# Kernel tuning notes

Measured on AMD Instinct MI355X. Metric: run time of the kernel, lower is better.

Reference implementation:

```python
import jax, jax.numpy as jnp
import numpy as np
from jax import lax

B, DIM, H, W = 4, 128, 56, 56
NH, NG = 4, 2
CG = DIM // NG   # group channels (64)
HC = DIM // NH   # head channels (32)
KS = 7
ORF = 2.0        # offset_range_factor
EPS = 1e-5

def setup_inputs() -> dict:
    key = jax.random.key(0)
    ks = jax.random.split(key, 8)
    s = 0.05
    def rn(k, shp):
        return jax.random.normal(k, shp, jnp.float32) * s
    return {
        "x":    jax.random.normal(ks[0], (B, DIM, H, W), jnp.float32),
        "dw_w": rn(ks[1], (CG, 1, KS, KS)),   # depthwise conv weight
        "dw_b": jnp.zeros((CG,), jnp.float32),
        "ln_g": jnp.ones((CG,), jnp.float32),
        "ln_b": jnp.zeros((CG,), jnp.float32),
        "off_w": rn(ks[2], (2, CG)),          # 1x1 conv to 2 offset channels, no bias
        "q_w": rn(ks[3], (DIM, DIM)), "q_b": jnp.zeros((DIM,), jnp.float32),
        "k_w": rn(ks[4], (DIM, DIM)), "k_b": jnp.zeros((DIM,), jnp.float32),
        "v_w": rn(ks[5], (DIM, DIM)), "v_b": jnp.zeros((DIM,), jnp.float32),
        "o_w": rn(ks[6], (DIM, DIM)), "o_b": jnp.zeros((DIM,), jnp.float32),
    }

def _grid_sample_bilinear(img, grid):
    # img [N,C,Hi,Wi]; grid [N,Ho,Wo,2] with (x,y) in [-1,1]; align_corners=True, zero padding
    N, C, Hi, Wi = img.shape
    Ho, Wo = grid.shape[1], grid.shape[2]
    gx = (grid[..., 0] + 1.0) * 0.5 * (Wi - 1)
    gy = (grid[..., 1] + 1.0) * 0.5 * (Hi - 1)
    x0 = jnp.floor(gx); y0 = jnp.floor(gy)
    wx1 = gx - x0; wx0 = 1.0 - wx1
    wy1 = gy - y0; wy0 = 1.0 - wy1
    flat = img.reshape(N, C, Hi * Wi)
    def corner(xi, yi, w):
        valid = (xi >= 0) & (xi <= Wi - 1) & (yi >= 0) & (yi <= Hi - 1)
        xc = jnp.clip(xi, 0, Wi - 1).astype(jnp.int32)
        yc = jnp.clip(yi, 0, Hi - 1).astype(jnp.int32)
        idx = (yc * Wi + xc).reshape(N, 1, Ho * Wo)
        vals = jnp.take_along_axis(flat, idx, axis=2)
        return vals * (w * valid).reshape(N, 1, Ho * Wo)
    out = (corner(x0, y0, wx0 * wy0) + corner(x0 + 1.0, y0, wx1 * wy0)
           + corner(x0, y0 + 1.0, wx0 * wy1) + corner(x0 + 1.0, y0 + 1.0, wx1 * wy1))
    return out.reshape(N, C, Ho, Wo)

def reference(x, dw_w, dw_b, ln_g, ln_b, off_w, q_w, q_b, k_w, k_b, v_w, v_b, o_w, o_b):
    Bx = x.shape[0]
    # q projection (1x1 conv)
    q = jnp.einsum('oc,bchw->bohw', q_w, x) + q_b[None, :, None, None]
    # offset branch: depthwise conv -> LayerNorm(channels) -> GELU -> 1x1 conv (2 ch)
    q_off = q.reshape(Bx * NG, CG, H, W)
    h = lax.conv_general_dilated(q_off, dw_w, (1, 1), [(KS // 2, KS // 2)] * 2,
                                 feature_group_count=CG,
                                 dimension_numbers=('NCHW', 'OIHW', 'NCHW'))
    h = h + dw_b[None, :, None, None]
    hn = jnp.moveaxis(h, 1, -1)                       # [BG,H,W,CG]
    mu = hn.mean(-1, keepdims=True)
    var = ((hn - mu) ** 2).mean(-1, keepdims=True)
    hn = (hn - mu) * lax.rsqrt(var + EPS) * ln_g + ln_b
    hn = jax.nn.gelu(hn, approximate=False)
    off = jnp.einsum('pc,bhwc->bphw', off_w, hn)      # [BG,2,Hk,Wk], p=(y,x)
    Hk, Wk = off.shape[2], off.shape[3]
    n = Hk * Wk
    rng = jnp.array([1.0 / Hk, 1.0 / Wk], jnp.float32).reshape(1, 2, 1, 1)
    off = jnp.tanh(off) * rng * ORF
    off = jnp.moveaxis(off, 1, -1)                    # [BG,Hk,Wk,2]
    # normalized reference points (y,x)
    ry = (jnp.arange(Hk, dtype=jnp.float32) + 0.5) / Hk * 2.0 - 1.0
    rx = (jnp.arange(Wk, dtype=jnp.float32) + 0.5) / Wk * 2.0 - 1.0
    ref = jnp.stack(jnp.meshgrid(ry, rx, indexing='ij'), -1)  # [Hk,Wk,2]
    pos = off + ref[None]
    # deformable gather: grid_sample expects (x,y)
    xs = _grid_sample_bilinear(x.reshape(Bx * NG, CG, H, W), pos[..., ::-1])
    xs = xs.reshape(Bx, DIM, n)                       # group-major == channel layout
    k = jnp.einsum('oc,bcn->bon', k_w, xs) + k_b[None, :, None]
    v = jnp.einsum('oc,bcn->bon', v_w, xs) + v_b[None, :, None]
    qh = q.reshape(Bx * NH, HC, H * W)
    kh = k.reshape(Bx * NH, HC, n)
    vh = v.reshape(Bx * NH, HC, n)
    attn = jnp.einsum('bcm,bcn->bmn', qh, kh) * (HC ** -0.5)
    attn = jax.nn.softmax(attn, axis=2)
    out = jnp.einsum('bmn,bcn->bcm', attn, vh).reshape(Bx, DIM, H, W)
    return jnp.einsum('oc,bchw->bohw', o_w, out) + o_b[None, :, None, None]
```

## Files before the change

### kernel.cpp

```cpp
#include <hip/hip_runtime.h>
#include <hip/hip_bf16.h>

#define HW 3136

typedef short s16x8 __attribute__((ext_vector_type(8)));
typedef float f32x4 __attribute__((ext_vector_type(4)));
typedef unsigned short us4 __attribute__((ext_vector_type(4)));
typedef unsigned short us8 __attribute__((ext_vector_type(8)));

__device__ inline unsigned short f2bf(float f) {
  union { float f; unsigned int u; } v; v.f = f;
  unsigned int r = v.u + 0x7fff + ((v.u >> 16) & 1);
  return (unsigned short)(r >> 16);
}
__device__ inline float bf2f(unsigned short b) {
  union { unsigned int u; float f; } v; v.u = (unsigned int)b << 16;
  return v.f;
}

__global__ __launch_bounds__(256) void wconv_kernel(
    const float* __restrict__ w0, const float* __restrict__ w1,
    const float* __restrict__ w2, const float* __restrict__ w3,
    unsigned short* __restrict__ o0, unsigned short* __restrict__ o1,
    unsigned short* __restrict__ o2, unsigned short* __restrict__ o3h,
    unsigned short* __restrict__ o3l) {
  int i = blockIdx.x * 256 + threadIdx.x;
  int y = blockIdx.y;
  if (y < 3) {
    const float* s = (y == 0) ? w0 : (y == 1) ? w1 : w2;
    unsigned short* d = (y == 0) ? o0 : (y == 1) ? o1 : o2;
    d[i] = f2bf(s[i]);
  } else {
    float x = w3[i];
    unsigned short hi = f2bf(x);
    o3h[i] = hi;
    o3l[i] = f2bf(x - bf2f(hi));
  }
}

__global__ __launch_bounds__(128) void gemm_q_kernel(
    const float* __restrict__ x, const unsigned short* __restrict__ Wq,
    const float* __restrict__ bias, float* __restrict__ Outf,
    unsigned short* __restrict__ Outb) {
  int by = blockIdx.y;
  int b = by >> 1, oh = by & 1;
  int t = threadIdx.x;
  int w = t >> 6, l = t & 63;
  int lq = l & 15, h = l >> 4;
  int p = blockIdx.x * 32 + w * 16 + lq;

  union S8 { s16x8 v; unsigned short u[8]; };
  S8 bfr[4];
  const float* xs = x + (size_t)b * 128 * HW + p;
  #pragma unroll
  for (int k = 0; k < 4; ++k)
    #pragma unroll
    for (int j = 0; j < 8; ++j)
      bfr[k].u[j] = f2bf(xs[(size_t)(k * 32 + h * 8 + j) * HW]);

  f32x4 acc[4] = {};
  #pragma unroll
  for (int k = 0; k < 4; ++k) {
    #pragma unroll
    for (int ot = 0; ot < 4; ++ot) {
      int og = oh * 4 + ot;
      s16x8 af = *(const s16x8*)&Wq[(size_t)(og * 16 + lq) * 128 + k * 32 + h * 8];
      acc[ot] = __builtin_amdgcn_mfma_f32_16x16x32_bf16(af, bfr[k].v, acc[ot], 0, 0, 0);
    }
  }

  size_t cb = (size_t)b * 128 * HW;
  #pragma unroll
  for (int ot = 0; ot < 4; ++ot) {
    int og = oh * 4 + ot;
    float4 bv = *(const float4*)&bias[og * 16 + h * 4];
    float r[4] = {acc[ot][0] + bv.x, acc[ot][1] + bv.y,
                  acc[ot][2] + bv.z, acc[ot][3] + bv.w};
    #pragma unroll
    for (int i = 0; i < 4; ++i)
      Outf[cb + (size_t)(og * 16 + h * 4 + i) * HW + p] = r[i];
    const float S = 0.25503968151135f;
    us4 rb;
    #pragma unroll
    for (int i = 0; i < 4; ++i) rb[i] = f2bf(r[i] * S);
    *(us4*)&Outb[((size_t)b * HW + p) * 128 + og * 16 + h * 4] = rb;
  }
}

__global__ __launch_bounds__(128) void gemm_kv_kernel(
    const unsigned short* __restrict__ InT, const unsigned short* __restrict__ Wk,
    const unsigned short* __restrict__ Wv, const float* __restrict__ k_b,
    const float* __restrict__ v_b, unsigned short* __restrict__ kbT,
    unsigned short* __restrict__ vb) {
  int by = blockIdx.y;
  int b = by >> 1, oh = by & 1;
  int t = threadIdx.x;
  int w = t >> 6, l = t & 63;
  int lq = l & 15, h = l >> 4;
  int p = blockIdx.x * 32 + w * 16 + lq;

  s16x8 bfr[4];
  const unsigned short* bsrc = InT + ((size_t)b * HW + p) * 128 + h * 8;
  #pragma unroll
  for (int k = 0; k < 4; ++k) bfr[k] = *(const s16x8*)&bsrc[k * 32];

  {
    f32x4 acc[4] = {};
    #pragma unroll
    for (int k = 0; k < 4; ++k) {
      #pragma unroll
      for (int ot = 0; ot < 4; ++ot) {
        int og = oh * 4 + ot;
        s16x8 af = *(const s16x8*)&Wk[(size_t)(og * 16 + lq) * 128 + k * 32 + h * 8];
        acc[ot] = __builtin_amdgcn_mfma_f32_16x16x32_bf16(af, bfr[k], acc[ot], 0, 0, 0);
      }
    }
    #pragma unroll
    for (int ot = 0; ot < 4; ++ot) {
      int og = oh * 4 + ot;
      float4 bv = *(const float4*)&k_b[og * 16 + h * 4];
      us4 rb;
      #pragma unroll
      for (int i = 0; i < 4; ++i) rb[i] = f2bf(acc[ot][i] + bv[i]);
      *(us4*)&kbT[((size_t)b * HW + p) * 128 + og * 16 + h * 4] = rb;
    }
  }
  {
    f32x4 acc[4] = {};
    #pragma unroll
    for (int k = 0; k < 4; ++k) {
      #pragma unroll
      for (int ot = 0; ot < 4; ++ot) {
        int og = oh * 4 + ot;
        s16x8 af = *(const s16x8*)&Wv[(size_t)(og * 16 + lq) * 128 + k * 32 + h * 8];
        acc[ot] = __builtin_amdgcn_mfma_f32_16x16x32_bf16(af, bfr[k], acc[ot], 0, 0, 0);
      }
    }
    size_t cb = (size_t)b * 128 * HW;
    #pragma unroll
    for (int ot = 0; ot < 4; ++ot) {
      int og = oh * 4 + ot;
      float4 bv = *(const float4*)&v_b[og * 16 + h * 4];
      #pragma unroll
      for (int i = 0; i < 4; ++i)
        vb[cb + (size_t)(og * 16 + h * 4 + i) * HW + p] = f2bf(acc[ot][i] + bv[i]);
    }
  }
}

__global__ __launch_bounds__(128) void o_gemm_kernel(
    const unsigned short* __restrict__ AHi, const unsigned short* __restrict__ ALo,
    const unsigned short* __restrict__ WHi, const unsigned short* __restrict__ WLo,
    const float* __restrict__ bias, float* __restrict__ Outf) {
  int by = blockIdx.y;
  int b = by >> 1, oh = by & 1;
  int t = threadIdx.x;
  int w = t >> 6, l = t & 63;
  int lq = l & 15, h = l >> 4;
  int p = blockIdx.x * 32 + w * 16 + lq;

  s16x8 bH[4], bL[4];
  const unsigned short* bsH = AHi + ((size_t)b * HW + p) * 128 + h * 8;
  const unsigned short* bsL = ALo + ((size_t)b * HW + p) * 128 + h * 8;
  #pragma unroll
  for (int k = 0; k < 4; ++k) {
    bH[k] = *(const s16x8*)&bsH[k * 32];
    bL[k] = *(const s16x8*)&bsL[k * 32];
  }

  f32x4 acc[4] = {};
  #pragma unroll
  for (int k = 0; k < 4; ++k) {
    #pragma unroll
    for (int ot = 0; ot < 4; ++ot) {
      int og = oh * 4 + ot;
      size_t wi = (size_t)(og * 16 + lq) * 128 + k * 32 + h * 8;
      s16x8 aH = *(const s16x8*)&WHi[wi];
      s16x8 aL = *(const s16x8*)&WLo[wi];
      acc[ot] = __builtin_amdgcn_mfma_f32_16x16x32_bf16(aH, bH[k], acc[ot], 0, 0, 0);
      acc[ot] = __builtin_amdgcn_mfma_f32_16x16x32_bf16(aH, bL[k], acc[ot], 0, 0, 0);
      acc[ot] = __builtin_amdgcn_mfma_f32_16x16x32_bf16(aL, bH[k], acc[ot], 0, 0, 0);
    }
  }

  size_t cb = (size_t)b * 128 * HW;
  #pragma unroll
  for (int ot = 0; ot < 4; ++ot) {
    int og = oh * 4 + ot;
    float4 bv = *(const float4*)&bias[og * 16 + h * 4];
    #pragma unroll
    for (int i = 0; i < 4; ++i)
      Outf[cb + (size_t)(og * 16 + h * 4 + i) * HW + p] = acc[ot][i] + bv[i];
  }
}

__global__ __launch_bounds__(1024) void offset_kernel(
    const float* __restrict__ q, const float* __restrict__ dw_w,
    const float* __restrict__ dw_b, const float* __restrict__ ln_g,
    const float* __restrict__ ln_b, const float* __restrict__ off_w,
    float* __restrict__ pos) {
  __shared__ float vs[64][65];
  __shared__ float mu_s[64], rs_s[64];
  __shared__ float part[16][64][2];
  int bg = blockIdx.x, h = blockIdx.y;
  int t = threadIdx.x;
  int w = t & 63;
  int cq = t >> 6;
  int b = bg >> 1, g = bg & 1;
  const float* qb = q + ((size_t)b * 128 + (size_t)g * 64) * HW;

  #pragma unroll
  for (int i = 0; i < 4; ++i) {
    int c = cq * 4 + i;
    float acc = dw_b[c];
    const float* qc = qb + (size_t)c * HW;
    const float* wc = dw_w + c * 49;
    #pragma unroll
    for (int ky = 0; ky < 7; ++ky) {
      int y = h + ky - 3;
      if (y >= 0 && y < 56) {
        #pragma unroll
        for (int kx = 0; kx < 7; ++kx) {
          int xx = w + kx - 3;
          if (xx >= 0 && xx < 56)
            acc += qc[y * 56 + xx] * wc[ky * 7 + kx];
        }
      }
    }
    vs[c][w] = acc;
  }
  __syncthreads();

  if (cq == 0) {
    float sum = 0.f;
    #pragma unroll 8
    for (int c = 0; c < 64; ++c) sum += vs[c][w];
    float mu = sum * 0.015625f;
    float var = 0.f;
    #pragma unroll 8
    for (int c = 0; c < 64; ++c) { float d = vs[c][w] - mu; var += d * d; }
    mu_s[w] = mu;
    rs_s[w] = rsqrtf(var * 0.015625f + 1e-5f);
  }
  __syncthreads();

  {
    float mu = mu_s[w], rstd = rs_s[w];
    float oy = 0.f, ox = 0.f;
    #pragma unroll
    for (int i = 0; i < 4; ++i) {
      int c = cq * 4 + i;
      float hn = (vs[c][w] - mu) * rstd * ln_g[c] + ln_b[c];
      hn = 0.5f * hn * (1.f + erff(hn * 0.70710678118654752f));
      oy += off_w[c] * hn;
      ox += off_w[64 + c] * hn;
    }
    part[cq][w][0] = oy;
    part[cq][w][1] = ox;
  }
  __syncthreads();

  if (cq == 0 && w < 56) {
    float oy = 0.f, ox = 0.f;
    #pragma unroll
    for (int pw = 0; pw < 16; ++pw) {
      oy += part[pw][w][0];
      ox += part[pw][w][1];
    }
    float py = tanhf(oy) * (2.0f / 56.f) + ((h + 0.5f) * (2.f / 56.f) - 1.f);
    float px = tanhf(ox) * (2.0f / 56.f) + ((w + 0.5f) * (2.f / 56.f) - 1.f);
    int idx = bg * HW + h * 56 + w;
    pos[idx * 2 + 0] = (px + 1.f) * 0.5f * 55.f;
    pos[idx * 2 + 1] = (py + 1.f) * 0.5f * 55.f;
  }
}

__global__ __launch_bounds__(256) void sample_kernel(
    const float* __restrict__ x, const float* __restrict__ pos,
    unsigned short* __restrict__ xsT) {
  int t = threadIdx.x;
  int p = blockIdx.x * 64 + (t & 63);
  int cg = t >> 6;
  int bg = p / HW, pp = p % HW;
  int b = bg >> 1, g = bg & 1;
  float gx = pos[2 * p], gy = pos[2 * p + 1];
  float x0f = floorf(gx), y0f = floorf(gy);
  float wx1 = gx - x0f, wx0 = 1.f - wx1;
  float wy1 = gy - y0f, wy0 = 1.f - wy1;
  int x0 = (int)x0f, y0 = (int)y0f;
  int x1 = x0 + 1, y1 = y0 + 1;
  float vx0 = (x0 >= 0 && x0 < 56) ? 1.f : 0.f;
  float vx1 = (x1 >= 0 && x1 < 56) ? 1.f : 0.f;
  float vy0 = (y0 >= 0 && y0 < 56) ? 1.f : 0.f;
  float vy1 = (y1 >= 0 && y1 < 56) ? 1.f : 0.f;
  int xc0 = min(max(x0, 0), 55), xc1 = min(max(x1, 0), 55);
  int yc0 = min(max(y0, 0), 55), yc1 = min(max(y1, 0), 55);
  float w00 = wx0 * wy0 * vx0 * vy0, w10 = wx1 * wy0 * vx1 * vy0;
  float w01 = wx0 * wy1 * vx0 * vy1, w11 = wx1 * wy1 * vx1 * vy1;
  int i00 = yc0 * 56 + xc0, i10 = yc0 * 56 + xc1;
  int i01 = yc1 * 56 + xc0, i11 = yc1 * 56 + xc1;
  const float* xb = x + ((size_t)b * 128 + (size_t)g * 64 + cg * 16) * HW;
  unsigned short tmp[16];
  #pragma unroll 4
  for (int i = 0; i < 16; ++i) {
    const float* xc = xb + (size_t)i * HW;
    tmp[i] = f2bf(w00 * xc[i00] + w10 * xc[i10] + w01 * xc[i01] + w11 * xc[i11]);
  }
  unsigned short* dst = xsT + ((size_t)b * HW + pp) * 128 + g * 64 + cg * 16;
  *(us8*)&dst[0] = *(us8*)&tmp[0];
  *(us8*)&dst[8] = *(us8*)&tmp[8];
}

__global__ __launch_bounds__(128) void attn_mfma_kernel(
    const unsigned short* __restrict__ qT, const unsigned short* __restrict__ kT,
    const unsigned short* __restrict__ vbf, unsigned short* __restrict__ aoHi,
    unsigned short* __restrict__ aoLo) {
  __shared__ __align__(16) unsigned short Klds[2][64][40];
  __shared__ __align__(16) unsigned short Plds[2][2][16][68];
  const int KSTEP = 64 * 40;
  int bh = blockIdx.y;
  int b = bh >> 2, hd = bh & 3;
  int t = threadIdx.x;
  int w = t >> 6, l = t & 63;
  int lq = l & 15, h = l >> 4;
  int q0 = blockIdx.x * 64 + w * 32;
  size_t vbase = (size_t)bh * 32 * HW;

  union S8 { s16x8 v; long long q[2]; unsigned short u[8]; };

  S8 qf0, qf1;
  qf0.v = *(const s16x8*)&qT[((size_t)b * HW + q0 + lq) * 128 + hd * 32 + h * 8];
  qf1.v = *(const s16x8*)&qT[((size_t)b * HW + q0 + 16 + lq) * 128 + hd * 32 + h * 8];

  int srow = t >> 1, sseg = (t & 1) * 16;
  const unsigned short* ksrc =
      kT + ((size_t)b * HW + srow) * 128 + hd * 32 + sseg;
  unsigned short* kdst = &Klds[0][srow][sseg];

  const unsigned short* vl = vbf + vbase + (size_t)lq * HW + h * 8;

  f32x4 oacc0[2] = {{0.f, 0.f, 0.f, 0.f}, {0.f, 0.f, 0.f, 0.f}};
  f32x4 oacc1[2] = {{0.f, 0.f, 0.f, 0.f}, {0.f, 0.f, 0.f, 0.f}};
  float lsum0 = 0.f, lsum1 = 0.f;

  S8 kr0, kr1, vreg[4];
  kr0.v = *(const s16x8*)&ksrc[0];
  kr1.v = *(const s16x8*)&ksrc[8];
  *(s16x8*)&kdst[0] = kr0.v;
  *(s16x8*)&kdst[8] = kr1.v;
  kr0.v = *(const s16x8*)&ksrc[(size_t)64 * 128];
  kr1.v = *(const s16x8*)&ksrc[(size_t)64 * 128 + 8];
  #pragma unroll
  for (int c = 0; c < 2; ++c)
    #pragma unroll
    for (int n = 0; n < 2; ++n)
      vreg[c * 2 + n].v = *(const s16x8*)&vl[(size_t)(n * 16) * HW + c * 32];
  asm volatile("s_waitcnt lgkmcnt(0)" ::: "memory");
  __builtin_amdgcn_s_barrier();

  for (int tix = 0; tix < 49; ++tix) {
    int cur = tix & 1;
    int kbV = (tix + 1 < 49) ? (tix + 1) * 64 : 0;
    int kbK = (tix + 2 < 49) ? (tix + 2) * 64 : 3072;

    f32x4 st0[4], st1[4];
    #pragma unroll
    for (int tt = 0; tt < 4; ++tt) {
      S8 af;
      af.v = *(const s16x8*)&Klds[cur][tt * 16 + lq][h * 8];
      st0[tt] = __builtin_amdgcn_mfma_f32_16x16x32_bf16(
          af.v, qf0.v, (f32x4){0.f, 0.f, 0.f, 0.f}, 0, 0, 0);
      st1[tt] = __builtin_amdgcn_mfma_f32_16x16x32_bf16(
          af.v, qf1.v, (f32x4){0.f, 0.f, 0.f, 0.f}, 0, 0, 0);
    }

    #pragma unroll
    for (int tt = 0; tt < 4; ++tt) {
      float a0, a1, a2, a3, b0, b1, b2, b3;
      asm("v_exp_f32 %0, %1" : "=v"(a0) : "v"(st0[tt][0]));
      asm("v_exp_f32 %0, %1" : "=v"(a1) : "v"(st0[tt][1]));
      asm("v_exp_f32 %0, %1" : "=v"(a2) : "v"(st0[tt][2]));
      asm("v_exp_f32 %0, %1" : "=v"(a3) : "v"(st0[tt][3]));
      asm("v_exp_f32 %0, %1" : "=v"(b0) : "v"(st1[tt][0]));
      asm("v_exp_f32 %0, %1" : "=v"(b1) : "v"(st1[tt][1]));
      asm("v_exp_f32 %0, %1" : "=v"(b2) : "v"(st1[tt][2]));
      asm("v_exp_f32 %0, %1" : "=v"(b3) : "v"(st1[tt][3]));
      lsum0 += (a0 + a1) + (a2 + a3);
      lsum1 += (b0 + b1) + (b2 + b3);
      unsigned int lo0, hi0, lo1, hi1;
      asm("v_cvt_pk_bf16_f32 %0, %1, %2" : "=v"(lo0) : "v"(a0), "v"(a1));
      asm("v_cvt_pk_bf16_f32 %0, %1, %2" : "=v"(hi0) : "v"(a2), "v"(a3));
      asm("v_cvt_pk_bf16_f32 %0, %1, %2" : "=v"(lo1) : "v"(b0), "v"(b1));
      asm("v_cvt_pk_bf16_f32 %0, %1, %2" : "=v"(hi1) : "v"(b2), "v"(b3));
      unsigned long long pk0 = (unsigned long long)lo0 | ((unsigned long long)hi0 << 32);
      unsigned long long pk1 = (unsigned long long)lo1 | ((unsigned long long)hi1 << 32);
      *(unsigned long long*)&Plds[w][0][lq][tt * 16 + h * 4] = pk0;
      *(unsigned long long*)&Plds[w][1][lq][tt * 16 + h * 4] = pk1;
    }

    #pragma unroll
    for (int c = 0; c < 2; ++c) {
      S8 pf0, pf1;
      pf0.q[0] = *(const long long*)&Plds[w][0][lq][c * 32 + h * 8];
      pf0.q[1] = *(const long long*)&Plds[w][0][lq][c * 32 + h * 8 + 4];
      pf1.q[0] = *(const long long*)&Plds[w][1][lq][c * 32 + h * 8];
      pf1.q[1] = *(const long long*)&Plds[w][1][lq][c * 32 + h * 8 + 4];
      #pragma unroll
      for (int n = 0; n < 2; ++n) {
        oacc0[n] = __builtin_amdgcn_mfma_f32_16x16x32_bf16(
            vreg[c * 2 + n].v, pf0.v, oacc0[n], 0, 0, 0);
        oacc1[n] = __builtin_amdgcn_mfma_f32_16x16x32_bf16(
            vreg[c * 2 + n].v, pf1.v, oacc1[n], 0, 0, 0);
      }
    }

    #pragma unroll
    for (int c = 0; c < 2; ++c)
      #pragma unroll
      for (int n = 0; n < 2; ++n)
        vreg[c * 2 + n].v =
            *(const s16x8*)&vl[(size_t)(n * 16) * HW + kbV + c * 32];

    *(s16x8*)(kdst + (cur ^ 1) * KSTEP) = kr0.v;
    *(s16x8*)(kdst + (cur ^ 1) * KSTEP + 8) = kr1.v;
    kr0.v = *(const s16x8*)&ksrc[(size_t)kbK * 128];
    kr1.v = *(const s16x8*)&ksrc[(size_t)kbK * 128 + 8];

    asm volatile("s_waitcnt lgkmcnt(0)" ::: "memory");
    __builtin_amdgcn_s_barrier();
  }

  lsum0 += __shfl_xor(lsum0, 16);
  lsum0 += __shfl_xor(lsum0, 32);
  lsum1 += __shfl_xor(lsum1, 16);
  lsum1 += __shfl_xor(lsum1, 32);
  float inv0 = 1.f / lsum0;
  float inv1 = 1.f / lsum1;
  #pragma unroll
  for (int f = 0; f < 2; ++f) {
    float inv = f ? inv1 : inv0;
    f32x4* oacc = f ? oacc1 : oacc0;
    size_t obase = ((size_t)b * HW + q0 + f * 16 + lq) * 128 + hd * 32;
    #pragma unroll
    for (int n = 0; n < 2; ++n) {
      us4 rh, rl;
      #pragma unroll
      for (int r = 0; r < 4; ++r) {
        float v = oacc[n][r] * inv;
        unsigned short hi = f2bf(v);
        rh[r] = hi;
        rl[r] = f2bf(v - bf2f(hi));
      }
      *(us4*)&aoHi[obase + n * 16 + h * 4] = rh;
      *(us4*)&aoLo[obase + n * 16 + h * 4] = rl;
    }
  }
}

extern "C" void kernel_launch(void* const* d_in, const int* in_sizes, int n_in,
                              void* d_out, int out_size, void* d_ws, size_t ws_size,
                              hipStream_t stream) {
  const float* x    = (const float*)d_in[0];
  const float* dw_w = (const float*)d_in[1];
  const float* dw_b = (const float*)d_in[2];
  const float* ln_g = (const float*)d_in[3];
  const float* ln_b = (const float*)d_in[4];
  const float* offw = (const float*)d_in[5];
  const float* q_w  = (const float*)d_in[6];
  const float* q_b  = (const float*)d_in[7];
  const float* k_w  = (const float*)d_in[8];
  const float* k_b  = (const float*)d_in[9];
  const float* v_w  = (const float*)d_in[10];
  const float* v_b  = (const float*)d_in[11];
  const float* o_w  = (const float*)d_in[12];
  const float* o_b  = (const float*)d_in[13];

  const size_t NE = 1605632;
  float* ws  = (float*)d_ws;
  float* q   = ws;
  float* pos = q + NE;
  unsigned short* xsT  = (unsigned short*)(pos + 50176);
  unsigned short* qbT  = xsT + NE;
  unsigned short* kbT  = qbT + NE;
  unsigned short* vb   = kbT + NE;
  unsigned short* aoHi = vb + NE;
  unsigned short* aoLo = aoHi + NE;
  unsigned short* Wq   = aoLo + NE;
  unsigned short* Wk   = Wq + 16384;
  unsigned short* Wv   = Wk + 16384;
  unsigned short* WoH  = Wv + 16384;
  unsigned short* WoL  = WoH + 16384;
  float* out = (float*)d_out;

  wconv_kernel<<<dim3(64, 4), 256, 0, stream>>>(q_w, k_w, v_w, o_w,
                                                Wq, Wk, Wv, WoH, WoL);
  gemm_q_kernel<<<dim3(98, 8), 128, 0, stream>>>(x, Wq, q_b, q, qbT);
  offset_kernel<<<dim3(8, 56), 1024, 0, stream>>>(q, dw_w, dw_b, ln_g, ln_b, offw, pos);
  sample_kernel<<<dim3(392), 256, 0, stream>>>(x, pos, xsT);
  gemm_kv_kernel<<<dim3(98, 8), 128, 0, stream>>>(xsT, Wk, Wv, k_b, v_b, kbT, vb);
  attn_mfma_kernel<<<dim3(49, 16), 128, 0, stream>>>(qbT, kbT, vb, aoHi, aoLo);
  o_gemm_kernel<<<dim3(98, 8), 128, 0, stream>>>(aoHi, aoLo, WoH, WoL, o_b, out);
}
```

Baseline: 145.4 us.

## Split attention key range across two wave pairs and merge partial sums in LDS

The attention kernel now launches 256 threads per block. Two pairs of waves each process about half of the 49 key tiles for the same 64 queries, each pair with its own double-buffered K tile in LDS. At the end, one half writes its unnormalized output accumulators and row sums to shared memory, and the other half adds them, normalizes and stores the result. The aim is more waves in flight and a shorter serial loop per wave, which matters because the grid has only 784 blocks. The cost is more LDS, a merge step, and one wasted padded iteration where the second half has no valid tile.

```diff
diff --git a/kernel.cpp b/kernel.cpp
--- a/kernel.cpp
+++ b/kernel.cpp
@@ -311,19 +311,20 @@
   *(us8*)&dst[8] = *(us8*)&tmp[8];
 }
 
-__global__ __launch_bounds__(128) void attn_mfma_kernel(
+__global__ __launch_bounds__(256) void attn_mfma_kernel(
     const unsigned short* __restrict__ qT, const unsigned short* __restrict__ kT,
     const unsigned short* __restrict__ vbf, unsigned short* __restrict__ aoHi,
     unsigned short* __restrict__ aoLo) {
-  __shared__ __align__(16) unsigned short Klds[2][64][40];
-  __shared__ __align__(16) unsigned short Plds[2][2][16][68];
+  __shared__ __align__(16) unsigned short Klds[2][2][64][40];
+  __shared__ __align__(16) unsigned short Plds[4][2][16][68];
   const int KSTEP = 64 * 40;
   int bh = blockIdx.y;
   int b = bh >> 2, hd = bh & 3;
   int t = threadIdx.x;
   int w = t >> 6, l = t & 63;
+  int qg = w >> 1, kh = w & 1;
   int lq = l & 15, h = l >> 4;
-  int q0 = blockIdx.x * 64 + w * 32;
+  int q0 = blockIdx.x * 64 + qg * 32;
   size_t vbase = (size_t)bh * 32 * HW;
 
   union S8 { s16x8 v; long long q[2]; unsigned short u[8]; };
@@ -332,10 +333,11 @@
   qf0.v = *(const s16x8*)&qT[((size_t)b * HW + q0 + lq) * 128 + hd * 32 + h * 8];
   qf1.v = *(const s16x8*)&qT[((size_t)b * HW + q0 + 16 + lq) * 128 + hd * 32 + h * 8];
 
-  int srow = t >> 1, sseg = (t & 1) * 16;
+  int pid = qg * 64 + l;
+  int srow = pid >> 1, sseg = (pid & 1) * 16;
   const unsigned short* ksrc =
       kT + ((size_t)b * HW + srow) * 128 + hd * 32 + sseg;
-  unsigned short* kdst = &Klds[0][srow][sseg];
+  unsigned short* kdst = &Klds[kh][0][srow][sseg];
 
   const unsigned short* vl = vbf + vbase + (size_t)lq * HW + h * 8;
 
@@ -343,74 +345,84 @@
   f32x4 oacc1[2] = {{0.f, 0.f, 0.f, 0.f}, {0.f, 0.f, 0.f, 0.f}};
   float lsum0 = 0.f, lsum1 = 0.f;
 
+  int tbase = kh * 25;
+
   S8 kr0, kr1, vreg[4];
-  kr0.v = *(const s16x8*)&ksrc[0];
-  kr1.v = *(const s16x8*)&ksrc[8];
-  *(s16x8*)&kdst[0] = kr0.v;
-  *(s16x8*)&kdst[8] = kr1.v;
-  kr0.v = *(const s16x8*)&ksrc[(size_t)64 * 128];
-  kr1.v = *(const s16x8*)&ksrc[(size_t)64 * 128 + 8];
-  #pragma unroll
-  for (int c = 0; c < 2; ++c)
-    #pragma unroll
-    for (int n = 0; n < 2; ++n)
-      vreg[c * 2 + n].v = *(const s16x8*)&vl[(size_t)(n * 16) * HW + c * 32];
+  {
+    size_t o0 = (size_t)(tbase * 64) * 128;
+    kr0.v = *(const s16x8*)&ksrc[o0];
+    kr1.v = *(const s16x8*)&ksrc[o0 + 8];
+    *(s16x8*)&kdst[0] = kr0.v;
+    *(s16x8*)&kdst[8] = kr1.v;
+    size_t o1 = (size_t)(min(tbase + 1, 48) * 64) * 128;
+    kr0.v = *(const s16x8*)&ksrc[o1];
+    kr1.v = *(const s16x8*)&ksrc[o1 + 8];
+    #pragma unroll
+    for (int c = 0; c < 2; ++c)
+      #pragma unroll
+      for (int n = 0; n < 2; ++n)
+        vreg[c * 2 + n].v =
+            *(const s16x8*)&vl[(size_t)(n * 16) * HW + tbase * 64 + c * 32];
+  }
   asm volatile("s_waitcnt lgkmcnt(0)" ::: "memory");
   __builtin_amdgcn_s_barrier();
 
-  for (int tix = 0; tix < 49; ++tix) {
-    int cur = tix & 1;
-    int kbV = (tix + 1 < 49) ? (tix + 1) * 64 : 0;
-    int kbK = (tix + 2 < 49) ? (tix + 2) * 64 : 3072;
-
-    f32x4 st0[4], st1[4];
-    #pragma unroll
-    for (int tt = 0; tt < 4; ++tt) {
-      S8 af;
-      af.v = *(const s16x8*)&Klds[cur][tt * 16 + lq][h * 8];
-      st0[tt] = __builtin_amdgcn_mfma_f32_16x16x32_bf16(
-          af.v, qf0.v, (f32x4){0.f, 0.f, 0.f, 0.f}, 0, 0, 0);
-      st1[tt] = __builtin_amdgcn_mfma_f32_16x16x32_bf16(
-          af.v, qf1.v, (f32x4){0.f, 0.f, 0.f, 0.f}, 0, 0, 0);
-    }
-
-    #pragma unroll
-    for (int tt = 0; tt < 4; ++tt) {
-      float a0, a1, a2, a3, b0, b1, b2, b3;
-      asm("v_exp_f32 %0, %1" : "=v"(a0) : "v"(st0[tt][0]));
-      asm("v_exp_f32 %0, %1" : "=v"(a1) : "v"(st0[tt][1]));
-      asm("v_exp_f32 %0, %1" : "=v"(a2) : "v"(st0[tt][2]));
-      asm("v_exp_f32 %0, %1" : "=v"(a3) : "v"(st0[tt][3]));
-      asm("v_exp_f32 %0, %1" : "=v"(b0) : "v"(st1[tt][0]));
-      asm("v_exp_f32 %0, %1" : "=v"(b1) : "v"(st1[tt][1]));
-      asm("v_exp_f32 %0, %1" : "=v"(b2) : "v"(st1[tt][2]));
-      asm("v_exp_f32 %0, %1" : "=v"(b3) : "v"(st1[tt][3]));
-      lsum0 += (a0 + a1) + (a2 + a3);
-      lsum1 += (b0 + b1) + (b2 + b3);
-      unsigned int lo0, hi0, lo1, hi1;
-      asm("v_cvt_pk_bf16_f32 %0, %1, %2" : "=v"(lo0) : "v"(a0), "v"(a1));
-      asm("v_cvt_pk_bf16_f32 %0, %1, %2" : "=v"(hi0) : "v"(a2), "v"(a3));
-      asm("v_cvt_pk_bf16_f32 %0, %1, %2" : "=v"(lo1) : "v"(b0), "v"(b1));
-      asm("v_cvt_pk_bf16_f32 %0, %1, %2" : "=v"(hi1) : "v"(b2), "v"(b3));
-      unsigned long long pk0 = (unsigned long long)lo0 | ((unsigned long long)hi0 << 32);
-      unsigned long long pk1 = (unsigned long long)lo1 | ((unsigned long long)hi1 << 32);
-      *(unsigned long long*)&Plds[w][0][lq][tt * 16 + h * 4] = pk0;
-      *(unsigned long long*)&Plds[w][1][lq][tt * 16 + h * 4] = pk1;
-    }
-
-    #pragma unroll
-    for (int c = 0; c < 2; ++c) {
-      S8 pf0, pf1;
-      pf0.q[0] = *(const long long*)&Plds[w][0][lq][c * 32 + h * 8];
-      pf0.q[1] = *(const long long*)&Plds[w][0][lq][c * 32 + h * 8 + 4];
-      pf1.q[0] = *(const long long*)&Plds[w][1][lq][c * 32 + h * 8];
-      pf1.q[1] = *(const long long*)&Plds[w][1][lq][c * 32 + h * 8 + 4];
-      #pragma unroll
-      for (int n = 0; n < 2; ++n) {
-        oacc0[n] = __builtin_amdgcn_mfma_f32_16x16x32_bf16(
-            vreg[c * 2 + n].v, pf0.v, oacc0[n], 0, 0, 0);
-        oacc1[n] = __builtin_amdgcn_mfma_f32_16x16x32_bf16(
-            vreg[c * 2 + n].v, pf1.v, oacc1[n], 0, 0, 0);
+  for (int i = 0; i < 25; ++i) {
+    int cur = i & 1;
+    bool vld = (tbase + i) < 49;
+    int tV = min(tbase + i + 1, 48) * 64;
+    int tK = min(tbase + i + 2, 48) * 64;
+
+    if (vld) {
+      f32x4 st0[4], st1[4];
+      #pragma unroll
+      for (int tt = 0; tt < 4; ++tt) {
+        S8 af;
+        af.v = *(const s16x8*)&Klds[kh][cur][tt * 16 + lq][h * 8];
+        st0[tt] = __builtin_amdgcn_mfma_f32_16x16x32_bf16(
+            af.v, qf0.v, (f32x4){0.f, 0.f, 0.f, 0.f}, 0, 0, 0);
+        st1[tt] = __builtin_amdgcn_mfma_f32_16x16x32_bf16(
+            af.v, qf1.v, (f32x4){0.f, 0.f, 0.f, 0.f}, 0, 0, 0);
+      }
+
+      #pragma unroll
+      for (int tt = 0; tt < 4; ++tt) {
+        float a0, a1, a2, a3, b0, b1, b2, b3;
+        asm("v_exp_f32 %0, %1" : "=v"(a0) : "v"(st0[tt][0]));
+        asm("v_exp_f32 %0, %1" : "=v"(a1) : "v"(st0[tt][1]));
+        asm("v_exp_f32 %0, %1" : "=v"(a2) : "v"(st0[tt][2]));
+        asm("v_exp_f32 %0, %1" : "=v"(a3) : "v"(st0[tt][3]));
+        asm("v_exp_f32 %0, %1" : "=v"(b0) : "v"(st1[tt][0]));
+        asm("v_exp_f32 %0, %1" : "=v"(b1) : "v"(st1[tt][1]));
+        asm("v_exp_f32 %0, %1" : "=v"(b2) : "v"(st1[tt][2]));
+        asm("v_exp_f32 %0, %1" : "=v"(b3) : "v"(st1[tt][3]));
+        lsum0 += (a0 + a1) + (a2 + a3);
+        lsum1 += (b0 + b1) + (b2 + b3);
+        unsigned int lo0, hi0, lo1, hi1;
+        asm("v_cvt_pk_bf16_f32 %0, %1, %2" : "=v"(lo0) : "v"(a0), "v"(a1));
+        asm("v_cvt_pk_bf16_f32 %0, %1, %2" : "=v"(hi0) : "v"(a2), "v"(a3));
+        asm("v_cvt_pk_bf16_f32 %0, %1, %2" : "=v"(lo1) : "v"(b0), "v"(b1));
+        asm("v_cvt_pk_bf16_f32 %0, %1, %2" : "=v"(hi1) : "v"(b2), "v"(b3));
+        unsigned long long pk0 = (unsigned long long)lo0 | ((unsigned long long)hi0 << 32);
+        unsigned long long pk1 = (unsigned long long)lo1 | ((unsigned long long)hi1 << 32);
+        *(unsigned long long*)&Plds[w][0][lq][tt * 16 + h * 4] = pk0;
+        *(unsigned long long*)&Plds[w][1][lq][tt * 16 + h * 4] = pk1;
+      }
+
+      #pragma unroll
+      for (int c = 0; c < 2; ++c) {
+        S8 pf0, pf1;
+        pf0.q[0] = *(const long long*)&Plds[w][0][lq][c * 32 + h * 8];
+        pf0.q[1] = *(const long long*)&Plds[w][0][lq][c * 32 + h * 8 + 4];
+        pf1.q[0] = *(const long long*)&Plds[w][1][lq][c * 32 + h * 8];
+        pf1.q[1] = *(const long long*)&Plds[w][1][lq][c * 32 + h * 8 + 4];
+        #pragma unroll
+        for (int n = 0; n < 2; ++n) {
+          oacc0[n] = __builtin_amdgcn_mfma_f32_16x16x32_bf16(
+              vreg[c * 2 + n].v, pf0.v, oacc0[n], 0, 0, 0);
+          oacc1[n] = __builtin_amdgcn_mfma_f32_16x16x32_bf16(
+              vreg[c * 2 + n].v, pf1.v, oacc1[n], 0, 0, 0);
+        }
       }
     }
 
@@ -419,12 +431,12 @@
       #pragma unroll
       for (int n = 0; n < 2; ++n)
         vreg[c * 2 + n].v =
-            *(const s16x8*)&vl[(size_t)(n * 16) * HW + kbV + c * 32];
-
-    *(s16x8*)(kdst + (cur ^ 1) * KSTEP) = kr0.v;
-    *(s16x8*)(kdst + (cur ^ 1) * KSTEP + 8) = kr1.v;
-    kr0.v = *(const s16x8*)&ksrc[(size_t)kbK * 128];
-    kr1.v = *(const s16x8*)&ksrc[(size_t)kbK * 128 + 8];
+            *(const s16x8*)&vl[(size_t)(n * 16) * HW + tV + c * 32];
+
+    *(s16x8*)(kdst + ((i + 1) & 1) * KSTEP) = kr0.v;
+    *(s16x8*)(kdst + ((i + 1) & 1) * KSTEP + 8) = kr1.v;
+    kr0.v = *(const s16x8*)&ksrc[(size_t)tK * 128];
+    kr1.v = *(const s16x8*)&ksrc[(size_t)tK * 128 + 8];
 
     asm volatile("s_waitcnt lgkmcnt(0)" ::: "memory");
     __builtin_amdgcn_s_barrier();
@@ -434,25 +446,45 @@
   lsum0 += __shfl_xor(lsum0, 32);
   lsum1 += __shfl_xor(lsum1, 16);
   lsum1 += __shfl_xor(lsum1, 32);
-  float inv0 = 1.f / lsum0;
-  float inv1 = 1.f / lsum1;
-  #pragma unroll
-  for (int f = 0; f < 2; ++f) {
-    float inv = f ? inv1 : inv0;
-    f32x4* oacc = f ? oacc1 : oacc0;
-    size_t obase = ((size_t)b * HW + q0 + f * 16 + lq) * 128 + hd * 32;
-    #pragma unroll
-    for (int n = 0; n < 2; ++n) {
-      us4 rh, rl;
-      #pragma unroll
-      for (int r = 0; r < 4; ++r) {
-        float v = oacc[n][r] * inv;
-        unsigned short hi = f2bf(v);
-        rh[r] = hi;
-        rl[r] = f2bf(v - bf2f(hi));
-      }
-      *(us4*)&aoHi[obase + n * 16 + h * 4] = rh;
-      *(us4*)&aoLo[obase + n * 16 + h * 4] = rl;
+
+  float* fb = (float*)&Klds[0][0][0][0];
+  if (kh == 1) {
+    #pragma unroll
+    for (int f = 0; f < 2; ++f) {
+      f32x4* oacc = f ? oacc1 : oacc0;
+      #pragma unroll
+      for (int n = 0; n < 2; ++n)
+        *(f32x4*)&fb[((qg * 2 + f) * 2 + n) * 320 + lq * 20 + h * 4] = oacc[n];
+    }
+    if (h == 0) {
+      fb[2560 + qg * 32 + lq] = lsum0;
+      fb[2560 + qg * 32 + 16 + lq] = lsum1;
+    }
+  }
+  asm volatile("s_waitcnt lgkmcnt(0)" ::: "memory");
+  __builtin_amdgcn_s_barrier();
+
+  if (kh == 0) {
+    #pragma unroll
+    for (int f = 0; f < 2; ++f) {
+      float lsum = (f ? lsum1 : lsum0) + fb[2560 + qg * 32 + f * 16 + lq];
+      float inv = 1.f / lsum;
+      f32x4* oacc = f ? oacc1 : oacc0;
+      size_t obase = ((size_t)b * HW + q0 + f * 16 + lq) * 128 + hd * 32;
+      #pragma unroll
+      for (int n = 0; n < 2; ++n) {
+        f32x4 rem = *(const f32x4*)&fb[((qg * 2 + f) * 2 + n) * 320 + lq * 20 + h * 4];
+        us4 rh, rl;
+        #pragma unroll
+        for (int r = 0; r < 4; ++r) {
+          float v = (oacc[n][r] + rem[r]) * inv;
+          unsigned short hi = f2bf(v);
+          rh[r] = hi;
+          rl[r] = f2bf(v - bf2f(hi));
+        }
+        *(us4*)&aoHi[obase + n * 16 + h * 4] = rh;
+        *(us4*)&aoLo[obase + n * 16 + h * 4] = rl;
+      }
     }
   }
 }
@@ -498,6 +530,6 @@
   offset_kernel<<<dim3(8, 56), 1024, 0, stream>>>(q, dw_w, dw_b, ln_g, ln_b, offw, pos);
   sample_kernel<<<dim3(392), 256, 0, stream>>>(x, pos, xsT);
   gemm_kv_kernel<<<dim3(98, 8), 128, 0, stream>>>(xsT, Wk, Wv, k_b, v_b, kbT, vb);
-  attn_mfma_kernel<<<dim3(49, 16), 128, 0, stream>>>(qbT, kbT, vb, aoHi, aoLo);
+  attn_mfma_kernel<<<dim3(49, 16), 256, 0, stream>>>(qbT, kbT, vb, aoHi, aoLo);
   o_gemm_kernel<<<dim3(98, 8), 128, 0, stream>>>(aoHi, aoLo, WoH, WoL, o_b, out);
 }
```

New measurement: 151.4 us. 1.04x slower.

## Use single-wave attention blocks processing 64 queries without barriers

Applied to the files above, without the earlier changes.

The attention kernel now runs one 64-thread wave per block handling four 16-query fragments instead of two waves of two fragments each. Each wave loads the whole K tile row into LDS itself, so the per-iteration workgroup barrier and LDS wait are removed, and K/V fragments are reused across more queries. The trade-off is half as many waves in flight and higher register use for the larger accumulator set, which may reduce latency hiding.

```diff
diff --git a/kernel.cpp b/kernel.cpp
--- a/kernel.cpp
+++ b/kernel.cpp
@@ -311,106 +311,113 @@
   *(us8*)&dst[8] = *(us8*)&tmp[8];
 }
 
-__global__ __launch_bounds__(128) void attn_mfma_kernel(
+__global__ __launch_bounds__(64) void attn_mfma_kernel(
     const unsigned short* __restrict__ qT, const unsigned short* __restrict__ kT,
     const unsigned short* __restrict__ vbf, unsigned short* __restrict__ aoHi,
     unsigned short* __restrict__ aoLo) {
   __shared__ __align__(16) unsigned short Klds[2][64][40];
-  __shared__ __align__(16) unsigned short Plds[2][2][16][68];
+  __shared__ __align__(16) unsigned short Plds[4][16][68];
   const int KSTEP = 64 * 40;
   int bh = blockIdx.y;
   int b = bh >> 2, hd = bh & 3;
-  int t = threadIdx.x;
-  int w = t >> 6, l = t & 63;
+  int l = threadIdx.x;
   int lq = l & 15, h = l >> 4;
-  int q0 = blockIdx.x * 64 + w * 32;
+  int q0 = blockIdx.x * 64;
   size_t vbase = (size_t)bh * 32 * HW;
 
   union S8 { s16x8 v; long long q[2]; unsigned short u[8]; };
 
-  S8 qf0, qf1;
-  qf0.v = *(const s16x8*)&qT[((size_t)b * HW + q0 + lq) * 128 + hd * 32 + h * 8];
-  qf1.v = *(const s16x8*)&qT[((size_t)b * HW + q0 + 16 + lq) * 128 + hd * 32 + h * 8];
-
-  int srow = t >> 1, sseg = (t & 1) * 16;
-  const unsigned short* ksrc =
-      kT + ((size_t)b * HW + srow) * 128 + hd * 32 + sseg;
-  unsigned short* kdst = &Klds[0][srow][sseg];
+  S8 qf[4];
+  #pragma unroll
+  for (int f = 0; f < 4; ++f)
+    qf[f].v = *(const s16x8*)&qT[((size_t)b * HW + q0 + f * 16 + lq) * 128 +
+                                 hd * 32 + h * 8];
+
+  const unsigned short* ksrc = kT + ((size_t)b * HW + l) * 128 + hd * 32;
+  unsigned short* kdst = &Klds[0][l][0];
 
   const unsigned short* vl = vbf + vbase + (size_t)lq * HW + h * 8;
 
-  f32x4 oacc0[2] = {{0.f, 0.f, 0.f, 0.f}, {0.f, 0.f, 0.f, 0.f}};
-  f32x4 oacc1[2] = {{0.f, 0.f, 0.f, 0.f}, {0.f, 0.f, 0.f, 0.f}};
-  float lsum0 = 0.f, lsum1 = 0.f;
-
-  S8 kr0, kr1, vreg[4];
-  kr0.v = *(const s16x8*)&ksrc[0];
-  kr1.v = *(const s16x8*)&ksrc[8];
-  *(s16x8*)&kdst[0] = kr0.v;
-  *(s16x8*)&kdst[8] = kr1.v;
-  kr0.v = *(const s16x8*)&ksrc[(size_t)64 * 128];
-  kr1.v = *(const s16x8*)&ksrc[(size_t)64 * 128 + 8];
+  f32x4 oacc[4][2] = {};
+  float lsum[4] = {0.f, 0.f, 0.f, 0.f};
+
+  S8 kreg[4], vreg[4];
+  #pragma unroll
+  for (int i = 0; i < 4; ++i) kreg[i].v = *(const s16x8*)&ksrc[i * 8];
+  #pragma unroll
+  for (int i = 0; i < 4; ++i) *(s16x8*)&kdst[i * 8] = kreg[i].v;
+  #pragma unroll
+  for (int i = 0; i < 4; ++i)
+    kreg[i].v = *(const s16x8*)&ksrc[(size_t)64 * 128 + i * 8];
   #pragma unroll
   for (int c = 0; c < 2; ++c)
     #pragma unroll
     for (int n = 0; n < 2; ++n)
       vreg[c * 2 + n].v = *(const s16x8*)&vl[(size_t)(n * 16) * HW + c * 32];
-  asm volatile("s_waitcnt lgkmcnt(0)" ::: "memory");
-  __builtin_amdgcn_s_barrier();
 
   for (int tix = 0; tix < 49; ++tix) {
     int cur = tix & 1;
     int kbV = (tix + 1 < 49) ? (tix + 1) * 64 : 0;
     int kbK = (tix + 2 < 49) ? (tix + 2) * 64 : 3072;
 
-    f32x4 st0[4], st1[4];
-    #pragma unroll
-    for (int tt = 0; tt < 4; ++tt) {
-      S8 af;
-      af.v = *(const s16x8*)&Klds[cur][tt * 16 + lq][h * 8];
-      st0[tt] = __builtin_amdgcn_mfma_f32_16x16x32_bf16(
-          af.v, qf0.v, (f32x4){0.f, 0.f, 0.f, 0.f}, 0, 0, 0);
-      st1[tt] = __builtin_amdgcn_mfma_f32_16x16x32_bf16(
-          af.v, qf1.v, (f32x4){0.f, 0.f, 0.f, 0.f}, 0, 0, 0);
-    }
-
-    #pragma unroll
-    for (int tt = 0; tt < 4; ++tt) {
-      float a0, a1, a2, a3, b0, b1, b2, b3;
-      asm("v_exp_f32 %0, %1" : "=v"(a0) : "v"(st0[tt][0]));
-      asm("v_exp_f32 %0, %1" : "=v"(a1) : "v"(st0[tt][1]));
-      asm("v_exp_f32 %0, %1" : "=v"(a2) : "v"(st0[tt][2]));
-      asm("v_exp_f32 %0, %1" : "=v"(a3) : "v"(st0[tt][3]));
-      asm("v_exp_f32 %0, %1" : "=v"(b0) : "v"(st1[tt][0]));
-      asm("v_exp_f32 %0, %1" : "=v"(b1) : "v"(st1[tt][1]));
-      asm("v_exp_f32 %0, %1" : "=v"(b2) : "v"(st1[tt][2]));
-      asm("v_exp_f32 %0, %1" : "=v"(b3) : "v"(st1[tt][3]));
-      lsum0 += (a0 + a1) + (a2 + a3);
-      lsum1 += (b0 + b1) + (b2 + b3);
-      unsigned int lo0, hi0, lo1, hi1;
-      asm("v_cvt_pk_bf16_f32 %0, %1, %2" : "=v"(lo0) : "v"(a0), "v"(a1));
-      asm("v_cvt_pk_bf16_f32 %0, %1, %2" : "=v"(hi0) : "v"(a2), "v"(a3));
-      asm("v_cvt_pk_bf16_f32 %0, %1, %2" : "=v"(lo1) : "v"(b0), "v"(b1));
-      asm("v_cvt_pk_bf16_f32 %0, %1, %2" : "=v"(hi1) : "v"(b2), "v"(b3));
-      unsigned long long pk0 = (unsigned long long)lo0 | ((unsigned long long)hi0 << 32);
-      unsigned long long pk1 = (unsigned long long)lo1 | ((unsigned long long)hi1 << 32);
-      *(unsigned long long*)&Plds[w][0][lq][tt * 16 + h * 4] = pk0;
-      *(unsigned long long*)&Plds[w][1][lq][tt * 16 + h * 4] = pk1;
+    S8 af[4];
+    #pragma unroll
+    for (int tt = 0; tt < 4; ++tt)
+      af[tt].v = *(const s16x8*)&Klds[cur][tt * 16 + lq][h * 8];
+
+    #pragma unroll
+    for (int i = 0; i < 4; ++i)
+      *(s16x8*)(kdst + (cur ^ 1) * KSTEP + i * 8) = kreg[i].v;
+    #pragma unroll
+    for (int i = 0; i < 4; ++i)
+      kreg[i].v = *(const s16x8*)&ksrc[(size_t)kbK * 128 + i * 8];
+
+    #pragma unroll
+    for (int pr = 0; pr < 2; ++pr) {
+      f32x4 stA[4], stB[4];
+      #pragma unroll
+      for (int tt = 0; tt < 4; ++tt) {
+        stA[tt] = __builtin_amdgcn_mfma_f32_16x16x32_bf16(
+            af[tt].v, qf[pr * 2].v, (f32x4){0.f, 0.f, 0.f, 0.f}, 0, 0, 0);
+        stB[tt] = __builtin_amdgcn_mfma_f32_16x16x32_bf16(
+            af[tt].v, qf[pr * 2 + 1].v, (f32x4){0.f, 0.f, 0.f, 0.f}, 0, 0, 0);
+      }
+      #pragma unroll
+      for (int tt = 0; tt < 4; ++tt) {
+        float a0, a1, a2, a3, b0, b1, b2, b3;
+        asm("v_exp_f32 %0, %1" : "=v"(a0) : "v"(stA[tt][0]));
+        asm("v_exp_f32 %0, %1" : "=v"(a1) : "v"(stA[tt][1]));
+        asm("v_exp_f32 %0, %1" : "=v"(a2) : "v"(stA[tt][2]));
+        asm("v_exp_f32 %0, %1" : "=v"(a3) : "v"(stA[tt][3]));
+        asm("v_exp_f32 %0, %1" : "=v"(b0) : "v"(stB[tt][0]));
+        asm("v_exp_f32 %0, %1" : "=v"(b1) : "v"(stB[tt][1]));
+        asm("v_exp_f32 %0, %1" : "=v"(b2) : "v"(stB[tt][2]));
+        asm("v_exp_f32 %0, %1" : "=v"(b3) : "v"(stB[tt][3]));
+        lsum[pr * 2] += (a0 + a1) + (a2 + a3);
+        lsum[pr * 2 + 1] += (b0 + b1) + (b2 + b3);
+        unsigned int lo0, hi0, lo1, hi1;
+        asm("v_cvt_pk_bf16_f32 %0, %1, %2" : "=v"(lo0) : "v"(a0), "v"(a1));
+        asm("v_cvt_pk_bf16_f32 %0, %1, %2" : "=v"(hi0) : "v"(a2), "v"(a3));
+        asm("v_cvt_pk_bf16_f32 %0, %1, %2" : "=v"(lo1) : "v"(b0), "v"(b1));
+        asm("v_cvt_pk_bf16_f32 %0, %1, %2" : "=v"(hi1) : "v"(b2), "v"(b3));
+        unsigned long long pk0 = (unsigned long long)lo0 | ((unsigned long long)hi0 << 32);
+        unsigned long long pk1 = (unsigned long long)lo1 | ((unsigned long long)hi1 << 32);
+        *(unsigned long long*)&Plds[pr * 2][lq][tt * 16 + h * 4] = pk0;
+        *(unsigned long long*)&Plds[pr * 2 + 1][lq][tt * 16 + h * 4] = pk1;
+      }
     }
 
     #pragma unroll
     for (int c = 0; c < 2; ++c) {
-      S8 pf0, pf1;
-      pf0.q[0] = *(const long long*)&Plds[w][0][lq][c * 32 + h * 8];
-      pf0.q[1] = *(const long long*)&Plds[w][0][lq][c * 32 + h * 8 + 4];
-      pf1.q[0] = *(const long long*)&Plds[w][1][lq][c * 32 + h * 8];
-      pf1.q[1] = *(const long long*)&Plds[w][1][lq][c * 32 + h * 8 + 4];
-      #pragma unroll
-      for (int n = 0; n < 2; ++n) {
-        oacc0[n] = __builtin_amdgcn_mfma_f32_16x16x32_bf16(
-            vreg[c * 2 + n].v, pf0.v, oacc0[n], 0, 0, 0);
-        oacc1[n] = __builtin_amdgcn_mfma_f32_16x16x32_bf16(
-            vreg[c * 2 + n].v, pf1.v, oacc1[n], 0, 0, 0);
+      #pragma unroll
+      for (int f = 0; f < 4; ++f) {
+        S8 pf;
+        pf.q[0] = *(const long long*)&Plds[f][lq][c * 32 + h * 8];
+        pf.q[1] = *(const long long*)&Plds[f][lq][c * 32 + h * 8 + 4];
+        #pragma unroll
+        for (int n = 0; n < 2; ++n)
+          oacc[f][n] = __builtin_amdgcn_mfma_f32_16x16x32_bf16(
+              vreg[c * 2 + n].v, pf.v, oacc[f][n], 0, 0, 0);
       }
     }
 
@@ -420,33 +427,21 @@
       for (int n = 0; n < 2; ++n)
         vreg[c * 2 + n].v =
             *(const s16x8*)&vl[(size_t)(n * 16) * HW + kbV + c * 32];
-
-    *(s16x8*)(kdst + (cur ^ 1) * KSTEP) = kr0.v;
-    *(s16x8*)(kdst + (cur ^ 1) * KSTEP + 8) = kr1.v;
-    kr0.v = *(const s16x8*)&ksrc[(size_t)kbK * 128];
-    kr1.v = *(const s16x8*)&ksrc[(size_t)kbK * 128 + 8];
-
-    asm volatile("s_waitcnt lgkmcnt(0)" ::: "memory");
-    __builtin_amdgcn_s_barrier();
-  }
-
-  lsum0 += __shfl_xor(lsum0, 16);
-  lsum0 += __shfl_xor(lsum0, 32);
-  lsum1 += __shfl_xor(lsum1, 16);
-  lsum1 += __shfl_xor(lsum1, 32);
-  float inv0 = 1.f / lsum0;
-  float inv1 = 1.f / lsum1;
-  #pragma unroll
-  for (int f = 0; f < 2; ++f) {
-    float inv = f ? inv1 : inv0;
-    f32x4* oacc = f ? oacc1 : oacc0;
+  }
+
+  #pragma unroll
+  for (int f = 0; f < 4; ++f) {
+    float ls = lsum[f];
+    ls += __shfl_xor(ls, 16);
+    ls += __shfl_xor(ls, 32);
+    float inv = 1.f / ls;
     size_t obase = ((size_t)b * HW + q0 + f * 16 + lq) * 128 + hd * 32;
     #pragma unroll
     for (int n = 0; n < 2; ++n) {
       us4 rh, rl;
       #pragma unroll
       for (int r = 0; r < 4; ++r) {
-        float v = oacc[n][r] * inv;
+        float v = oacc[f][n][r] * inv;
         unsigned short hi = f2bf(v);
         rh[r] = hi;
         rl[r] = f2bf(v - bf2f(hi));
@@ -498,6 +493,6 @@
   offset_kernel<<<dim3(8, 56), 1024, 0, stream>>>(q, dw_w, dw_b, ln_g, ln_b, offw, pos);
   sample_kernel<<<dim3(392), 256, 0, stream>>>(x, pos, xsT);
   gemm_kv_kernel<<<dim3(98, 8), 128, 0, stream>>>(xsT, Wk, Wv, k_b, v_b, kbT, vb);
-  attn_mfma_kernel<<<dim3(49, 16), 128, 0, stream>>>(qbT, kbT, vb, aoHi, aoLo);
+  attn_mfma_kernel<<<dim3(49, 16), 64, 0, stream>>>(qbT, kbT, vb, aoHi, aoLo);
   o_gemm_kernel<<<dim3(98, 8), 128, 0, stream>>>(aoHi, aoLo, WoH, WoL, o_b, out);
 }
```

After: 152.8 us. 1.05x slower.
